# Performance work log

Hardware: AMD Instinct MI355X
Metric: run time of the kernel (lower is better)

## Reference

```python
import jax, jax.numpy as jnp
import numpy as np

T, B, E, H = 2048, 2, 1024, 16
HD = E // H
EPS = 1e-5


def setup_inputs() -> dict:
    key = jax.random.key(0)
    k1, k2, k3 = jax.random.split(key, 3)
    bound_in = float(np.sqrt(6.0 / (3 * E + E)))   # xavier_uniform for [3E,E]
    bound_out = float(np.sqrt(6.0 / (E + E)))      # xavier_uniform for [E,E]
    return {
        "query": jax.random.normal(k1, (T, B, E), dtype=jnp.float32),
        "gamma": jnp.ones((E,), dtype=jnp.float32),
        "beta": jnp.zeros((E,), dtype=jnp.float32),
        "in_proj_weight": jax.random.uniform(k2, (3 * E, E), jnp.float32, -bound_in, bound_in),
        "out_proj_weight": jax.random.uniform(k3, (E, E), jnp.float32, -bound_out, bound_out),
    }


def reference(query, gamma, beta, in_proj_weight, out_proj_weight):
    # LayerNorm over channel dim
    mean = jnp.mean(query, axis=-1, keepdims=True)
    var = jnp.mean(jnp.square(query - mean), axis=-1, keepdims=True)
    ln = (query - mean) * jax.lax.rsqrt(var + EPS) * gamma + beta  # [T,B,E]

    # Fused QKV projection (no bias): qkv = ln @ W^T, W: [3E, E]
    qkv = jnp.einsum("tbe,fe->tbf", ln, in_proj_weight)  # [T,B,3E]
    q, k, v = jnp.split(qkv, 3, axis=-1)
    q = q.reshape(T, B, H, HD) * (HD ** -0.5)
    k = k.reshape(T, B, H, HD)
    v = v.reshape(T, B, H, HD)

    # Attention: scores [B,H,T,T]
    scores = jnp.einsum("tbhd,sbhd->bhts", q, k)
    attn = jax.nn.softmax(scores, axis=-1)
    ctx = jnp.einsum("bhts,sbhd->tbhd", attn, v).reshape(T, B, E)

    # Output projection + residual add (dropout prob = 0)
    out = jnp.einsum("tbe,fe->tbf", ctx, out_proj_weight)
    return query + out
```

## Files before the change

kernel.cpp:

```cpp
#include <hip/hip_runtime.h>
#include <hip/hip_bf16.h>
#include <math.h>

#define T_DIM 2048
#define B_DIM 2
#define E_DIM 1024
#define H_DIM 16
#define HD_DIM 64
#define M_DIM (T_DIM * B_DIM)
#define BH_DIM (B_DIM * H_DIM)

using bf16x8 = __attribute__((ext_vector_type(8))) __bf16;
using u16x8  = __attribute__((ext_vector_type(8))) unsigned short;
using u16x4  = __attribute__((ext_vector_type(4))) unsigned short;
using f32x4  = __attribute__((ext_vector_type(4))) float;

static __device__ __forceinline__ unsigned short f2bf(float f) {
  unsigned u = __builtin_bit_cast(unsigned, f);
  u += 0x7fff + ((u >> 16) & 1);
  return (unsigned short)(u >> 16);
}

__device__ __forceinline__ void gload_lds16(const void* g, void* l) {
  __builtin_amdgcn_global_load_lds(
      (const __attribute__((address_space(1))) unsigned int*)g,
      (__attribute__((address_space(3))) unsigned int*)l, 16, 0, 0);
}

__global__ __launch_bounds__(256) void cast2_kernel(
    const float* __restrict__ in1, unsigned short* __restrict__ out1, int n1,
    const float* __restrict__ in2, unsigned short* __restrict__ out2, int n2) {
  int i = blockIdx.x * 256 + threadIdx.x;
  const float* in; unsigned short* out; int idx;
  if (i < n1) { in = in1; out = out1; idx = i; }
  else if (i < n1 + n2) { in = in2; out = out2; idx = i - n1; }
  else return;
  float4 v = ((const float4*)in)[idx];
  ushort4 o;
  o.x = f2bf(v.x); o.y = f2bf(v.y); o.z = f2bf(v.z); o.w = f2bf(v.w);
  ((ushort4*)out)[idx] = o;
}

__global__ __launch_bounds__(256) void ln_kernel(
    const float* __restrict__ q, const float* __restrict__ gamma,
    const float* __restrict__ beta, unsigned short* __restrict__ out) {
  int row = blockIdx.x;
  int tid = threadIdx.x;
  const float4* qr = (const float4*)(q + (size_t)row * E_DIM);
  float4 x = qr[tid];
  float s  = x.x + x.y + x.z + x.w;
  float ss = x.x * x.x + x.y * x.y + x.z * x.z + x.w * x.w;
#pragma unroll
  for (int off = 32; off >= 1; off >>= 1) {
    s  += __shfl_xor(s, off, 64);
    ss += __shfl_xor(ss, off, 64);
  }
  __shared__ float red[8];
  int wid = tid >> 6, lane = tid & 63;
  if (lane == 0) { red[wid] = s; red[4 + wid] = ss; }
  __syncthreads();
  s  = red[0] + red[1] + red[2] + red[3];
  ss = red[4] + red[5] + red[6] + red[7];
  float mean = s * (1.0f / E_DIM);
  float var  = ss * (1.0f / E_DIM) - mean * mean;
  float rstd = rsqrtf(var + 1e-5f);
  float4 g4 = ((const float4*)gamma)[tid];
  float4 b4 = ((const float4*)beta)[tid];
  ushort4 o;
  o.x = f2bf((x.x - mean) * rstd * g4.x + b4.x);
  o.y = f2bf((x.y - mean) * rstd * g4.y + b4.y);
  o.z = f2bf((x.z - mean) * rstd * g4.z + b4.z);
  o.w = f2bf((x.w - mean) * rstd * g4.w + b4.w);
  ((ushort4*)(out + (size_t)row * E_DIM))[tid] = o;
}

__global__ __launch_bounds__(256) void gemm0_kernel(
    const unsigned short* __restrict__ A, const unsigned short* __restrict__ Bw,
    unsigned short* __restrict__ out_qkv) {
  __shared__ alignas(16) unsigned short lA[128 * 32];
  __shared__ alignas(16) unsigned short lB[128 * 32];
  int tid = threadIdx.x;
  int wid = tid >> 6, lane = tid & 63;
  int wm = wid >> 1, wn = wid & 1;
  int g = lane >> 4, lr = lane & 15;
  int m0 = blockIdx.y * 128, n0 = blockIdx.x * 128;
  f32x4 acc[4][4] = {};

  for (int k0 = 0; k0 < E_DIM; k0 += 32) {
#pragma unroll
    for (int c = 0; c < 2; ++c) {
      int f16 = c * 256 + tid;
      int row = f16 >> 2, col8 = (f16 & 3) << 3;
      gload_lds16(A  + (size_t)(m0 + row) * E_DIM + k0 + col8,
                  lA + (size_t)(c * 256 + wid * 64) * 8);
      gload_lds16(Bw + (size_t)(n0 + row) * E_DIM + k0 + col8,
                  lB + (size_t)(c * 256 + wid * 64) * 8);
    }
    __syncthreads();
    bf16x8 af[4], bfr[4];
#pragma unroll
    for (int r = 0; r < 4; ++r) {
      af[r]  = *(const bf16x8*)(lA + (wm * 64 + r * 16 + lr) * 32 + g * 8);
      bfr[r] = *(const bf16x8*)(lB + (wn * 64 + r * 16 + lr) * 32 + g * 8);
    }
#pragma unroll
    for (int mr = 0; mr < 4; ++mr)
#pragma unroll
      for (int nr = 0; nr < 4; ++nr)
        acc[mr][nr] = __builtin_amdgcn_mfma_f32_16x16x32_bf16(
            af[mr], bfr[nr], acc[mr][nr], 0, 0, 0);
    __syncthreads();
  }

#pragma unroll
  for (int mr = 0; mr < 4; ++mr) {
#pragma unroll
    for (int nr = 0; nr < 4; ++nr) {
#pragma unroll
      for (int r = 0; r < 4; ++r) {
        int grow = m0 + wm * 64 + mr * 16 + g * 4 + r;
        int gcol = n0 + wn * 64 + nr * 16 + lr;
        int which = gcol >> 10, rem = gcol & 1023;
        int h = rem >> 6, d = rem & 63;
        int t = grow >> 1, b = grow & 1;
        out_qkv[(size_t)which * (BH_DIM * T_DIM * HD_DIM) +
                ((size_t)(b * H_DIM + h) * T_DIM + t) * HD_DIM + d] =
            f2bf(acc[mr][nr][r]);
      }
    }
  }
}

__global__ __launch_bounds__(256) void gemm1_kernel(
    const unsigned short* __restrict__ A, const unsigned short* __restrict__ Bw,
    const float* __restrict__ resid, float* __restrict__ out) {
  __shared__ alignas(16) unsigned short lA[128 * 32];
  __shared__ alignas(16) unsigned short lB[64 * 32];
  int tid = threadIdx.x;
  int wid = tid >> 6, lane = tid & 63;
  int g = lane >> 4, lr = lane & 15;
  int m0 = blockIdx.y * 128, n0 = blockIdx.x * 64;
  f32x4 acc[2][4] = {};

  for (int k0 = 0; k0 < E_DIM; k0 += 32) {
#pragma unroll
    for (int c = 0; c < 2; ++c) {
      int f16 = c * 256 + tid;
      int row = f16 >> 2, col8 = (f16 & 3) << 3;
      gload_lds16(A + (size_t)(m0 + row) * E_DIM + k0 + col8,
                  lA + (size_t)(c * 256 + wid * 64) * 8);
    }
    {
      int row = tid >> 2, col8 = (tid & 3) << 3;
      gload_lds16(Bw + (size_t)(n0 + row) * E_DIM + k0 + col8,
                  lB + (size_t)(wid * 64) * 8);
    }
    __syncthreads();
    bf16x8 af[2], bfr[4];
#pragma unroll
    for (int r = 0; r < 2; ++r)
      af[r] = *(const bf16x8*)(lA + (wid * 32 + r * 16 + lr) * 32 + g * 8);
#pragma unroll
    for (int r = 0; r < 4; ++r)
      bfr[r] = *(const bf16x8*)(lB + (r * 16 + lr) * 32 + g * 8);
#pragma unroll
    for (int mr = 0; mr < 2; ++mr)
#pragma unroll
      for (int nr = 0; nr < 4; ++nr)
        acc[mr][nr] = __builtin_amdgcn_mfma_f32_16x16x32_bf16(
            af[mr], bfr[nr], acc[mr][nr], 0, 0, 0);
    __syncthreads();
  }

#pragma unroll
  for (int mr = 0; mr < 2; ++mr) {
#pragma unroll
    for (int nr = 0; nr < 4; ++nr) {
#pragma unroll
      for (int r = 0; r < 4; ++r) {
        int grow = m0 + wid * 32 + mr * 16 + g * 4 + r;
        int gcol = n0 + nr * 16 + lr;
        size_t idx = (size_t)grow * E_DIM + gcol;
        out[idx] = resid[idx] + acc[mr][nr][r];
      }
    }
  }
}

__global__ __launch_bounds__(256) void transpose_v_kernel(
    const unsigned short* __restrict__ vb, unsigned short* __restrict__ vt) {
  __shared__ alignas(16) unsigned short tl[64 * 72];
  int tid = threadIdx.x;
  int bh = blockIdx.y, t0 = blockIdx.x * 64;
  const unsigned short* src = vb + ((size_t)bh * T_DIM + t0) * HD_DIM;
#pragma unroll
  for (int e = 0; e < 2; ++e) {
    int i8 = e * 256 + tid;
    int r = i8 >> 3;
    int c = (i8 & 7) * 8;
    int hsh = (r ^ (r >> 3)) & 7;
    bf16x8 v = *(const bf16x8*)(src + (size_t)r * HD_DIM + c);
    *(bf16x8*)(tl + r * 72 + (c ^ (hsh << 3))) = v;
  }
  __syncthreads();
  unsigned short* dst = vt + (size_t)bh * HD_DIM * T_DIM + t0;
#pragma unroll
  for (int e = 0; e < 2; ++e) {
    int i8 = e * 256 + tid;
    int d = i8 >> 3;
    int tc = (i8 & 7) * 8;
    u16x8 o;
#pragma unroll
    for (int j = 0; j < 8; ++j) {
      int p = tc + j;
      int ks = p >> 5, gg = (p >> 3) & 3, jl = p & 7;
      int r = (ks * 2 + (jl >> 2)) * 16 + gg * 4 + (jl & 3);
      int hsh = (r ^ (r >> 3)) & 7;
      o[j] = tl[r * 72 + (d ^ (hsh << 3))];
    }
    *(u16x8*)(dst + (size_t)d * T_DIM + tc) = o;
  }
}

__global__ __launch_bounds__(256) void attn_kernel(
    const unsigned short* __restrict__ qb, const unsigned short* __restrict__ kb,
    const unsigned short* __restrict__ vt, unsigned short* __restrict__ ctx) {
  __shared__ alignas(16) unsigned short lK[3][64 * 64];
  __shared__ alignas(16) unsigned short lV[3][64 * 64];
  int tid = threadIdx.x;
  int wid = tid >> 6, lane = tid & 63;
  int g = lane >> 4, lr = lane & 15;
  int f = blockIdx.x;
  int xcd = f & 7, rest = f >> 3;
  int bh = xcd + 8 * (rest & 3);
  int qt = rest >> 2;
  int b = bh >> 4, h = bh & 15;
  const size_t koff = (size_t)bh * T_DIM * HD_DIM;
  const size_t voff = (size_t)bh * HD_DIM * T_DIM;

  int srow = tid >> 3;
  int gch  = (tid & 7) ^ (srow & 7);
  const unsigned short* ks0 = kb + koff + (size_t)srow * HD_DIM + gch * 8;
  const unsigned short* vs0 = vt + voff + (size_t)srow * T_DIM + gch * 8;

#define STAGE_TILE(buf, kofs, vofs)                                            \
  do {                                                                         \
    gload_lds16(ks0 + (kofs),                 lK[buf] + wid * 512);            \
    gload_lds16(ks0 + (kofs) + 32 * HD_DIM,   lK[buf] + 2048 + wid * 512);     \
    gload_lds16(vs0 + (vofs),                 lV[buf] + wid * 512);            \
    gload_lds16(vs0 + (vofs) + (size_t)32 * T_DIM, lV[buf] + 2048 + wid * 512);\
  } while (0)

  bf16x8 qf[2][2];
  {
    const float QS = 0.125f * 1.44269504f;
#pragma unroll
    for (int qa = 0; qa < 2; ++qa) {
      int qrow = qt * 128 + wid * 32 + qa * 16 + lr;
#pragma unroll
      for (int ks = 0; ks < 2; ++ks) {
        bf16x8 raw = *(const bf16x8*)(qb + koff + (size_t)qrow * HD_DIM + ks * 32 + g * 8);
#pragma unroll
        for (int j = 0; j < 8; ++j) qf[qa][ks][j] = (__bf16)((float)raw[j] * QS);
      }
    }
  }

  bf16x8 onesf;
#pragma unroll
  for (int j = 0; j < 8; ++j) onesf[j] = (__bf16)1.0f;

  f32x4 accO[2][4] = {};
  f32x4 accS[2] = {};

  const int NT = T_DIM / 64;
  STAGE_TILE(0, 0, 0);

#define PROCESS(BUF, NBUF, TT, LAST)                                           \
  do {                                                                         \
    if (!(LAST)) {                                                             \
      size_t s1 = (size_t)((TT) + 1) * 64;                                     \
      STAGE_TILE(NBUF, s1 * HD_DIM, s1);                                       \
      asm volatile("s_waitcnt vmcnt(4)" ::: "memory");                         \
    } else {                                                                   \
      asm volatile("s_waitcnt vmcnt(0)" ::: "memory");                         \
    }                                                                          \
    __builtin_amdgcn_s_barrier();                                              \
    __builtin_amdgcn_sched_barrier(0);                                         \
    const unsigned short* Kc = lK[BUF];                                        \
    const unsigned short* Vc = lV[BUF];                                        \
    f32x4 s4[2][4];                                                            \
    __builtin_amdgcn_s_setprio(1);                                             \
    _Pragma("unroll")                                                          \
    for (int cf = 0; cf < 4; ++cf) {                                           \
      int row = cf * 16 + lr;                                                  \
      int sw = (row & 7) << 3;                                                 \
      bf16x8 k0 = *(const bf16x8*)(Kc + row * 64 + ((g * 8) ^ sw));            \
      bf16x8 k1 = *(const bf16x8*)(Kc + row * 64 + ((32 + g * 8) ^ sw));       \
      _Pragma("unroll")                                                        \
      for (int qa = 0; qa < 2; ++qa) {                                         \
        f32x4 s = {-8.0f, -8.0f, -8.0f, -8.0f};                                \
        s = __builtin_amdgcn_mfma_f32_16x16x32_bf16(k0, qf[qa][0], s, 0, 0, 0);\
        s = __builtin_amdgcn_mfma_f32_16x16x32_bf16(k1, qf[qa][1], s, 0, 0, 0);\
        s4[qa][cf] = s;                                                        \
      }                                                                        \
    }                                                                          \
    __builtin_amdgcn_s_setprio(0);                                             \
    bf16x8 pf[2][2];                                                           \
    _Pragma("unroll")                                                          \
    for (int qa = 0; qa < 2; ++qa)                                             \
      _Pragma("unroll")                                                        \
      for (int j = 0; j < 8; ++j) {                                            \
        pf[qa][0][j] = (__bf16)__builtin_amdgcn_exp2f(s4[qa][(j >> 2)][j & 3]);\
        pf[qa][1][j] = (__bf16)__builtin_amdgcn_exp2f(s4[qa][2 + (j >> 2)][j & 3]);\
      }                                                                        \
    __builtin_amdgcn_s_setprio(1);                                             \
    _Pragma("unroll")                                                          \
    for (int ks = 0; ks < 2; ++ks) {                                           \
      _Pragma("unroll")                                                        \
      for (int qa = 0; qa < 2; ++qa)                                           \
        accS[qa] = __builtin_amdgcn_mfma_f32_16x16x32_bf16(onesf, pf[qa][ks], accS[qa], 0, 0, 0); \
      _Pragma("unroll")                                                        \
      for (int df = 0; df < 4; ++df) {                                         \
        int row = df * 16 + lr;                                                \
        int sw = (row & 7) << 3;                                               \
        bf16x8 vf = *(const bf16x8*)(Vc + row * 64 + ((ks * 32 + g * 8) ^ sw));\
        _Pragma("unroll")                                                      \
        for (int qa = 0; qa < 2; ++qa)                                         \
          accO[qa][df] = __builtin_amdgcn_mfma_f32_16x16x32_bf16(vf, pf[qa][ks], accO[qa][df], 0, 0, 0); \
      }                                                                        \
    }                                                                          \
    __builtin_amdgcn_s_setprio(0);                                             \
  } while (0)

  for (int t3 = 0; t3 < 30; t3 += 3) {
    PROCESS(0, 1, t3 + 0, false);
    PROCESS(1, 2, t3 + 1, false);
    PROCESS(2, 0, t3 + 2, false);
  }
  PROCESS(0, 1, 30, false);
  PROCESS(1, 2, 31, true);
#undef PROCESS
#undef STAGE_TILE

  __syncthreads();
  unsigned short* sc = (unsigned short*)lK + wid * (32 * 72);
  float invl[2];
  invl[0] = 1.0f / accS[0][0];
  invl[1] = 1.0f / accS[1][0];
#pragma unroll
  for (int qa = 0; qa < 2; ++qa)
#pragma unroll
    for (int df = 0; df < 4; ++df)
#pragma unroll
      for (int r = 0; r < 4; ++r)
        sc[(qa * 16 + lr) * 72 + df * 16 + g * 4 + r] =
            f2bf(accO[qa][df][r] * invl[qa]);
  __syncthreads();
#pragma unroll
  for (int i = 0; i < 4; ++i) {
    int idx = i * 64 + lane;
    int row = idx >> 3, ch = idx & 7;
    u16x8 v8 = *(const u16x8*)(sc + row * 72 + ch * 8);
    int t = qt * 128 + wid * 32 + row;
    *(u16x8*)(&ctx[((size_t)t * B_DIM + b) * E_DIM + h * HD_DIM + ch * 8]) = v8;
  }
}

extern "C" void kernel_launch(void* const* d_in, const int* in_sizes, int n_in,
                              void* d_out, int out_size, void* d_ws, size_t ws_size,
                              hipStream_t stream) {
  const float* query = (const float*)d_in[0];
  const float* gamma = (const float*)d_in[1];
  const float* beta  = (const float*)d_in[2];
  const float* w_in  = (const float*)d_in[3];
  const float* w_out = (const float*)d_in[4];
  float* out = (float*)d_out;

  unsigned short* ws    = (unsigned short*)d_ws;
  unsigned short* ln    = ws;
  unsigned short* winb  = ln + (size_t)M_DIM * E_DIM;
  unsigned short* woutb = winb + (size_t)3 * E_DIM * E_DIM;
  unsigned short* qkv   = woutb + (size_t)E_DIM * E_DIM;

  unsigned short* qbuf = qkv;
  unsigned short* kbuf = qkv + (size_t)BH_DIM * T_DIM * HD_DIM;
  unsigned short* vbuf = kbuf + (size_t)BH_DIM * T_DIM * HD_DIM;
  unsigned short* vtb  = ln;
  unsigned short* ctx  = vbuf;

  cast2_kernel<<<dim3(4096), dim3(256), 0, stream>>>(
      w_in, winb, 3 * E_DIM * E_DIM / 4, w_out, woutb, E_DIM * E_DIM / 4);
  ln_kernel<<<dim3(M_DIM), dim3(256), 0, stream>>>(query, gamma, beta, ln);
  gemm0_kernel<<<dim3(3 * E_DIM / 128, M_DIM / 128), dim3(256), 0, stream>>>(
      ln, winb, qkv);
  transpose_v_kernel<<<dim3(T_DIM / 64, BH_DIM), dim3(256), 0, stream>>>(vbuf, vtb);
  attn_kernel<<<dim3(512), dim3(256), 0, stream>>>(qbuf, kbuf, vtb, ctx);
  gemm1_kernel<<<dim3(E_DIM / 64, M_DIM / 128), dim3(256), 0, stream>>>(
      ctx, woutb, query, out);
}
```

Before: 122.3 us.

## Split attention over key halves with reduce kernel; fuse V transpose into QKV GEMM

```diff
diff --git a/kernel.cpp b/kernel.cpp
--- a/kernel.cpp
+++ b/kernel.cpp
@@ -12,13 +12,15 @@
 
 using bf16x8 = __attribute__((ext_vector_type(8))) __bf16;
 using u16x8  = __attribute__((ext_vector_type(8))) unsigned short;
-using u16x4  = __attribute__((ext_vector_type(4))) unsigned short;
 using f32x4  = __attribute__((ext_vector_type(4))) float;
 
 static __device__ __forceinline__ unsigned short f2bf(float f) {
   unsigned u = __builtin_bit_cast(unsigned, f);
   u += 0x7fff + ((u >> 16) & 1);
   return (unsigned short)(u >> 16);
+}
+static __device__ __forceinline__ float bf2f(unsigned short x) {
+  return __builtin_bit_cast(float, (unsigned)x << 16);
 }
 
 __device__ __forceinline__ void gload_lds16(const void* g, void* l) {
@@ -76,7 +78,8 @@
 
 __global__ __launch_bounds__(256) void gemm0_kernel(
     const unsigned short* __restrict__ A, const unsigned short* __restrict__ Bw,
-    unsigned short* __restrict__ out_qkv) {
+    unsigned short* __restrict__ out_q, unsigned short* __restrict__ out_k,
+    unsigned short* __restrict__ out_vt) {
   __shared__ alignas(16) unsigned short lA[128 * 32];
   __shared__ alignas(16) unsigned short lB[128 * 32];
   int tid = threadIdx.x;
@@ -123,9 +126,19 @@
         int which = gcol >> 10, rem = gcol & 1023;
         int h = rem >> 6, d = rem & 63;
         int t = grow >> 1, b = grow & 1;
-        out_qkv[(size_t)which * (BH_DIM * T_DIM * HD_DIM) +
-                ((size_t)(b * H_DIM + h) * T_DIM + t) * HD_DIM + d] =
-            f2bf(acc[mr][nr][r]);
+        size_t bh = (size_t)(b * H_DIM + h);
+        unsigned short val = f2bf(acc[mr][nr][r]);
+        if (which == 0) {
+          out_q[(bh * T_DIM + t) * HD_DIM + d] = val;
+        } else if (which == 1) {
+          out_k[(bh * T_DIM + t) * HD_DIM + d] = val;
+        } else {
+          int tile = t >> 6, trow = t & 63;
+          int cf = trow >> 4, rr = trow & 15;
+          int ks2 = cf >> 1, jh = cf & 1, g2 = rr >> 2, jl = rr & 3;
+          int p = ks2 * 32 + g2 * 8 + jh * 4 + jl;
+          out_vt[bh * (HD_DIM * T_DIM) + (size_t)d * T_DIM + tile * 64 + p] = val;
+        }
       }
     }
   }
@@ -187,61 +200,29 @@
   }
 }
 
-__global__ __launch_bounds__(256) void transpose_v_kernel(
-    const unsigned short* __restrict__ vb, unsigned short* __restrict__ vt) {
-  __shared__ alignas(16) unsigned short tl[64 * 72];
-  int tid = threadIdx.x;
-  int bh = blockIdx.y, t0 = blockIdx.x * 64;
-  const unsigned short* src = vb + ((size_t)bh * T_DIM + t0) * HD_DIM;
-#pragma unroll
-  for (int e = 0; e < 2; ++e) {
-    int i8 = e * 256 + tid;
-    int r = i8 >> 3;
-    int c = (i8 & 7) * 8;
-    int hsh = (r ^ (r >> 3)) & 7;
-    bf16x8 v = *(const bf16x8*)(src + (size_t)r * HD_DIM + c);
-    *(bf16x8*)(tl + r * 72 + (c ^ (hsh << 3))) = v;
-  }
-  __syncthreads();
-  unsigned short* dst = vt + (size_t)bh * HD_DIM * T_DIM + t0;
-#pragma unroll
-  for (int e = 0; e < 2; ++e) {
-    int i8 = e * 256 + tid;
-    int d = i8 >> 3;
-    int tc = (i8 & 7) * 8;
-    u16x8 o;
-#pragma unroll
-    for (int j = 0; j < 8; ++j) {
-      int p = tc + j;
-      int ks = p >> 5, gg = (p >> 3) & 3, jl = p & 7;
-      int r = (ks * 2 + (jl >> 2)) * 16 + gg * 4 + (jl & 3);
-      int hsh = (r ^ (r >> 3)) & 7;
-      o[j] = tl[r * 72 + (d ^ (hsh << 3))];
-    }
-    *(u16x8*)(dst + (size_t)d * T_DIM + tc) = o;
-  }
-}
-
 __global__ __launch_bounds__(256) void attn_kernel(
     const unsigned short* __restrict__ qb, const unsigned short* __restrict__ kb,
-    const unsigned short* __restrict__ vt, unsigned short* __restrict__ ctx) {
-  __shared__ alignas(16) unsigned short lK[3][64 * 64];
-  __shared__ alignas(16) unsigned short lV[3][64 * 64];
+    const unsigned short* __restrict__ vt, unsigned short* __restrict__ pO,
+    float* __restrict__ pS) {
+  __shared__ alignas(16) unsigned short lK[2][64 * 64];
+  __shared__ alignas(16) unsigned short lV[2][64 * 64];
   int tid = threadIdx.x;
   int wid = tid >> 6, lane = tid & 63;
   int g = lane >> 4, lr = lane & 15;
   int f = blockIdx.x;
   int xcd = f & 7, rest = f >> 3;
   int bh = xcd + 8 * (rest & 3);
-  int qt = rest >> 2;
-  int b = bh >> 4, h = bh & 15;
+  int qt = (rest >> 2) & 15;
+  int s  = (rest >> 6) & 1;
   const size_t koff = (size_t)bh * T_DIM * HD_DIM;
   const size_t voff = (size_t)bh * HD_DIM * T_DIM;
 
   int srow = tid >> 3;
   int gch  = (tid & 7) ^ (srow & 7);
-  const unsigned short* ks0 = kb + koff + (size_t)srow * HD_DIM + gch * 8;
-  const unsigned short* vs0 = vt + voff + (size_t)srow * T_DIM + gch * 8;
+  const unsigned short* ks0 = kb + koff +
+      ((size_t)(s * 1024) + srow) * HD_DIM + gch * 8;
+  const unsigned short* vs0 = vt + voff +
+      (size_t)srow * T_DIM + s * 1024 + gch * 8;
 
 #define STAGE_TILE(buf, kofs, vofs)                                            \
   do {                                                                         \
@@ -273,19 +254,19 @@
   f32x4 accO[2][4] = {};
   f32x4 accS[2] = {};
 
-  const int NT = T_DIM / 64;
   STAGE_TILE(0, 0, 0);
 
-#define PROCESS(BUF, NBUF, TT, LAST)                                           \
+#define PROCESS(BUF, TT, LAST)                                                 \
   do {                                                                         \
+    __builtin_amdgcn_s_barrier();            \
     if (!(LAST)) {                                                             \
       size_t s1 = (size_t)((TT) + 1) * 64;                                     \
-      STAGE_TILE(NBUF, s1 * HD_DIM, s1);                                       \
+      STAGE_TILE((BUF) ^ 1, s1 * HD_DIM, s1);                                  \
       asm volatile("s_waitcnt vmcnt(4)" ::: "memory");                         \
     } else {                                                                   \
       asm volatile("s_waitcnt vmcnt(0)" ::: "memory");                         \
     }                                                                          \
-    __builtin_amdgcn_s_barrier();                                              \
+    __builtin_amdgcn_s_barrier();              \
     __builtin_amdgcn_sched_barrier(0);                                         \
     const unsigned short* Kc = lK[BUF];                                        \
     const unsigned short* Vc = lV[BUF];                                        \
@@ -333,38 +314,67 @@
     __builtin_amdgcn_s_setprio(0);                                             \
   } while (0)
 
-  for (int t3 = 0; t3 < 30; t3 += 3) {
-    PROCESS(0, 1, t3 + 0, false);
-    PROCESS(1, 2, t3 + 1, false);
-    PROCESS(2, 0, t3 + 2, false);
-  }
-  PROCESS(0, 1, 30, false);
-  PROCESS(1, 2, 31, true);
+  for (int t2 = 0; t2 < 16; t2 += 2) {
+    PROCESS(0, t2, false);
+    PROCESS(1, t2 + 1, t2 + 1 == 15);
+  }
 #undef PROCESS
 #undef STAGE_TILE
 
+  unsigned short* pOb = pO + (size_t)((s * 32 + bh) * 16 + qt) * (64 * 128);
+#pragma unroll
+  for (int qa = 0; qa < 2; ++qa)
+#pragma unroll
+    for (int df = 0; df < 4; ++df)
+#pragma unroll
+      for (int r = 0; r < 4; ++r)
+        pOb[(df * 16 + g * 4 + r) * 128 + wid * 32 + qa * 16 + lr] =
+            f2bf(accO[qa][df][r]);
+  if (g == 0) {
+    float* pSb = pS + (size_t)((s * 32 + bh) * 16 + qt) * 128;
+#pragma unroll
+    for (int qa = 0; qa < 2; ++qa)
+      pSb[wid * 32 + qa * 16 + lr] = accS[qa][0];
+  }
+}
+
+__global__ __launch_bounds__(256) void reduce_kernel(
+    const unsigned short* __restrict__ pO, const float* __restrict__ pS,
+    unsigned short* __restrict__ ctx) {
+  __shared__ float lo[64][65];
+  __shared__ float ls[64];
+  int tid = threadIdx.x;
+  int bq = blockIdx.x;
+  int bh = bq & 31, qt2 = bq >> 5;
+  int b = bh >> 4, h = bh & 15;
+  int qt = qt2 >> 1, half = qt2 & 1;
+  size_t base0 = (size_t)((0 * 32 + bh) * 16 + qt) * 8192 + half * 64;
+  size_t base1 = (size_t)((1 * 32 + bh) * 16 + qt) * 8192 + half * 64;
+  int d = tid >> 2, c = (tid & 3) * 16;
+  u16x8 a0 = *(const u16x8*)(pO + base0 + d * 128 + c);
+  u16x8 a1 = *(const u16x8*)(pO + base0 + d * 128 + c + 8);
+  u16x8 b0 = *(const u16x8*)(pO + base1 + d * 128 + c);
+  u16x8 b1 = *(const u16x8*)(pO + base1 + d * 128 + c + 8);
+#pragma unroll
+  for (int j = 0; j < 8; ++j) {
+    lo[d][c + j]     = bf2f(a0[j]) + bf2f(b0[j]);
+    lo[d][c + 8 + j] = bf2f(a1[j]) + bf2f(b1[j]);
+  }
+  if (tid < 64)
+    ls[tid] = pS[(size_t)((0 * 32 + bh) * 16 + qt) * 128 + half * 64 + tid] +
+              pS[(size_t)((1 * 32 + bh) * 16 + qt) * 128 + half * 64 + tid];
   __syncthreads();
-  unsigned short* sc = (unsigned short*)lK + wid * (32 * 72);
-  float invl[2];
-  invl[0] = 1.0f / accS[0][0];
-  invl[1] = 1.0f / accS[1][0];
-#pragma unroll
-  for (int qa = 0; qa < 2; ++qa)
-#pragma unroll
-    for (int df = 0; df < 4; ++df)
-#pragma unroll
-      for (int r = 0; r < 4; ++r)
-        sc[(qa * 16 + lr) * 72 + df * 16 + g * 4 + r] =
-            f2bf(accO[qa][df][r] * invl[qa]);
-  __syncthreads();
-#pragma unroll
-  for (int i = 0; i < 4; ++i) {
-    int idx = i * 64 + lane;
-    int row = idx >> 3, ch = idx & 7;
-    u16x8 v8 = *(const u16x8*)(sc + row * 72 + ch * 8);
-    int t = qt * 128 + wid * 32 + row;
-    *(u16x8*)(&ctx[((size_t)t * B_DIM + b) * E_DIM + h * HD_DIM + ch * 8]) = v8;
-  }
+  int q = tid >> 2, dc = tid & 3;
+  float inv = 1.0f / ls[q];
+  u16x8 o0, o1;
+#pragma unroll
+  for (int k = 0; k < 8; ++k) {
+    o0[k] = f2bf(lo[dc * 16 + k][q] * inv);
+    o1[k] = f2bf(lo[dc * 16 + 8 + k][q] * inv);
+  }
+  size_t row = ((size_t)(qt2 * 64 + q) * B_DIM + b) * E_DIM + h * HD_DIM + dc * 16;
+  *(u16x8*)(ctx + row)     = o0;
+  *(u16x8*)(ctx + row + 8) = o1;
 }
 
 extern "C" void kernel_launch(void* const* d_in, const int* in_sizes, int n_in,
@@ -379,23 +389,22 @@
 
   unsigned short* ws    = (unsigned short*)d_ws;
   unsigned short* ln    = ws;
-  unsigned short* winb  = ln + (size_t)M_DIM * E_DIM;
-  unsigned short* woutb = winb + (size_t)3 * E_DIM * E_DIM;
-  unsigned short* qkv   = woutb + (size_t)E_DIM * E_DIM;
-
-  unsigned short* qbuf = qkv;
-  unsigned short* kbuf = qkv + (size_t)BH_DIM * T_DIM * HD_DIM;
-  unsigned short* vbuf = kbuf + (size_t)BH_DIM * T_DIM * HD_DIM;
-  unsigned short* vtb  = ln;
-  unsigned short* ctx  = vbuf;
+  unsigned short* winb  = ln    + (size_t)M_DIM * E_DIM;
+  unsigned short* woutb = winb  + (size_t)3 * E_DIM * E_DIM;
+  unsigned short* qbuf  = woutb + (size_t)E_DIM * E_DIM;
+  unsigned short* kbuf  = qbuf  + (size_t)BH_DIM * T_DIM * HD_DIM;
+  unsigned short* vtb   = kbuf  + (size_t)BH_DIM * T_DIM * HD_DIM;
+  unsigned short* pO    = vtb   + (size_t)BH_DIM * HD_DIM * T_DIM;
+  float*          pS    = (float*)(pO + (size_t)2 * BH_DIM * 16 * 64 * 128);
+  unsigned short* ctx   = ln;
 
   cast2_kernel<<<dim3(4096), dim3(256), 0, stream>>>(
       w_in, winb, 3 * E_DIM * E_DIM / 4, w_out, woutb, E_DIM * E_DIM / 4);
   ln_kernel<<<dim3(M_DIM), dim3(256), 0, stream>>>(query, gamma, beta, ln);
   gemm0_kernel<<<dim3(3 * E_DIM / 128, M_DIM / 128), dim3(256), 0, stream>>>(
-      ln, winb, qkv);
-  transpose_v_kernel<<<dim3(T_DIM / 64, BH_DIM), dim3(256), 0, stream>>>(vbuf, vtb);
-  attn_kernel<<<dim3(512), dim3(256), 0, stream>>>(qbuf, kbuf, vtb, ctx);
+      ln, winb, qbuf, kbuf, vtb);
+  attn_kernel<<<dim3(1024), dim3(256), 0, stream>>>(qbuf, kbuf, vtb, pO, pS);
+  reduce_kernel<<<dim3(1024), dim3(256), 0, stream>>>(pO, pS, ctx);
   gemm1_kernel<<<dim3(E_DIM / 64, M_DIM / 128), dim3(256), 0, stream>>>(
       ctx, woutb, query, out);
 }
```

Result: slower. 149.2 us (+22.0%).

## Software-pipeline QK^T of next tile with PV of current tile; merge prep kernels

Applied to the files above, without the earlier changes.

```diff
diff --git a/kernel.cpp b/kernel.cpp
--- a/kernel.cpp
+++ b/kernel.cpp
@@ -12,7 +12,6 @@
 
 using bf16x8 = __attribute__((ext_vector_type(8))) __bf16;
 using u16x8  = __attribute__((ext_vector_type(8))) unsigned short;
-using u16x4  = __attribute__((ext_vector_type(4))) unsigned short;
 using f32x4  = __attribute__((ext_vector_type(4))) float;
 
 static __device__ __forceinline__ unsigned short f2bf(float f) {
@@ -27,25 +26,26 @@
       (__attribute__((address_space(3))) unsigned int*)l, 16, 0, 0);
 }
 
-__global__ __launch_bounds__(256) void cast2_kernel(
-    const float* __restrict__ in1, unsigned short* __restrict__ out1, int n1,
-    const float* __restrict__ in2, unsigned short* __restrict__ out2, int n2) {
-  int i = blockIdx.x * 256 + threadIdx.x;
-  const float* in; unsigned short* out; int idx;
-  if (i < n1) { in = in1; out = out1; idx = i; }
-  else if (i < n1 + n2) { in = in2; out = out2; idx = i - n1; }
-  else return;
-  float4 v = ((const float4*)in)[idx];
-  ushort4 o;
-  o.x = f2bf(v.x); o.y = f2bf(v.y); o.z = f2bf(v.z); o.w = f2bf(v.w);
-  ((ushort4*)out)[idx] = o;
-}
-
-__global__ __launch_bounds__(256) void ln_kernel(
+__global__ __launch_bounds__(256) void prep_kernel(
     const float* __restrict__ q, const float* __restrict__ gamma,
-    const float* __restrict__ beta, unsigned short* __restrict__ out) {
-  int row = blockIdx.x;
+    const float* __restrict__ beta, unsigned short* __restrict__ ln_out,
+    const float* __restrict__ w1, unsigned short* __restrict__ o1, int n1,
+    const float* __restrict__ w2, unsigned short* __restrict__ o2, int n2) {
+  int blk = blockIdx.x;
   int tid = threadIdx.x;
+  if (blk >= M_DIM) {
+    int i = (blk - M_DIM) * 256 + tid;
+    const float* in; unsigned short* out; int idx;
+    if (i < n1) { in = w1; out = o1; idx = i; }
+    else if (i < n1 + n2) { in = w2; out = o2; idx = i - n1; }
+    else return;
+    float4 v = ((const float4*)in)[idx];
+    ushort4 o;
+    o.x = f2bf(v.x); o.y = f2bf(v.y); o.z = f2bf(v.z); o.w = f2bf(v.w);
+    ((ushort4*)out)[idx] = o;
+    return;
+  }
+  int row = blk;
   const float4* qr = (const float4*)(q + (size_t)row * E_DIM);
   float4 x = qr[tid];
   float s  = x.x + x.y + x.z + x.w;
@@ -71,7 +71,7 @@
   o.y = f2bf((x.y - mean) * rstd * g4.y + b4.y);
   o.z = f2bf((x.z - mean) * rstd * g4.z + b4.z);
   o.w = f2bf((x.w - mean) * rstd * g4.w + b4.w);
-  ((ushort4*)(out + (size_t)row * E_DIM))[tid] = o;
+  ((ushort4*)(ln_out + (size_t)row * E_DIM))[tid] = o;
 }
 
 __global__ __launch_bounds__(256) void gemm0_kernel(
@@ -272,25 +272,11 @@
 
   f32x4 accO[2][4] = {};
   f32x4 accS[2] = {};
-
-  const int NT = T_DIM / 64;
-  STAGE_TILE(0, 0, 0);
-
-#define PROCESS(BUF, NBUF, TT, LAST)                                           \
+  f32x4 s4c[2][4];
+
+#define QK_TILE(BUF, S4)                                                       \
   do {                                                                         \
-    if (!(LAST)) {                                                             \
-      size_t s1 = (size_t)((TT) + 1) * 64;                                     \
-      STAGE_TILE(NBUF, s1 * HD_DIM, s1);                                       \
-      asm volatile("s_waitcnt vmcnt(4)" ::: "memory");                         \
-    } else {                                                                   \
-      asm volatile("s_waitcnt vmcnt(0)" ::: "memory");                         \
-    }                                                                          \
-    __builtin_amdgcn_s_barrier();                                              \
-    __builtin_amdgcn_sched_barrier(0);                                         \
     const unsigned short* Kc = lK[BUF];                                        \
-    const unsigned short* Vc = lV[BUF];                                        \
-    f32x4 s4[2][4];                                                            \
-    __builtin_amdgcn_s_setprio(1);                                             \
     _Pragma("unroll")                                                          \
     for (int cf = 0; cf < 4; ++cf) {                                           \
       int row = cf * 16 + lr;                                                  \
@@ -302,45 +288,75 @@
         f32x4 s = {-8.0f, -8.0f, -8.0f, -8.0f};                                \
         s = __builtin_amdgcn_mfma_f32_16x16x32_bf16(k0, qf[qa][0], s, 0, 0, 0);\
         s = __builtin_amdgcn_mfma_f32_16x16x32_bf16(k1, qf[qa][1], s, 0, 0, 0);\
-        s4[qa][cf] = s;                                                        \
+        S4[qa][cf] = s;                                                        \
       }                                                                        \
     }                                                                          \
-    __builtin_amdgcn_s_setprio(0);                                             \
+  } while (0)
+
+  STAGE_TILE(0, 0, 0);
+  STAGE_TILE(1, (size_t)64 * HD_DIM, 64);
+  asm volatile("s_waitcnt vmcnt(4)" ::: "memory");
+  __builtin_amdgcn_s_barrier();
+  __builtin_amdgcn_sched_barrier(0);
+  QK_TILE(0, s4c);
+
+#define PROCESS(B0, B1, B2, TT, STG, QKN)                                      \
+  do {                                                                         \
+    asm volatile("s_waitcnt vmcnt(0)" ::: "memory");                           \
+    __builtin_amdgcn_s_barrier();                                              \
+    __builtin_amdgcn_sched_barrier(0);                                         \
+    if (STG) {                                                                 \
+      size_t s2 = (size_t)((TT) + 2) * 64;                                     \
+      STAGE_TILE(B2, s2 * HD_DIM, s2);                                         \
+    }                                                                          \
+    __builtin_amdgcn_s_setprio(1);                                             \
+    f32x4 s4n[2][4];                                                           \
+    if (QKN) QK_TILE(B1, s4n);                                                 \
     bf16x8 pf[2][2];                                                           \
     _Pragma("unroll")                                                          \
     for (int qa = 0; qa < 2; ++qa)                                             \
       _Pragma("unroll")                                                        \
       for (int j = 0; j < 8; ++j) {                                            \
-        pf[qa][0][j] = (__bf16)__builtin_amdgcn_exp2f(s4[qa][(j >> 2)][j & 3]);\
-        pf[qa][1][j] = (__bf16)__builtin_amdgcn_exp2f(s4[qa][2 + (j >> 2)][j & 3]);\
+        pf[qa][0][j] = (__bf16)__builtin_amdgcn_exp2f(s4c[qa][(j >> 2)][j & 3]);\
+        pf[qa][1][j] = (__bf16)__builtin_amdgcn_exp2f(s4c[qa][2 + (j >> 2)][j & 3]);\
       }                                                                        \
-    __builtin_amdgcn_s_setprio(1);                                             \
-    _Pragma("unroll")                                                          \
-    for (int ks = 0; ks < 2; ++ks) {                                           \
+    {                                                                          \
+      const unsigned short* Vc = lV[B0];                                       \
       _Pragma("unroll")                                                        \
-      for (int qa = 0; qa < 2; ++qa)                                           \
-        accS[qa] = __builtin_amdgcn_mfma_f32_16x16x32_bf16(onesf, pf[qa][ks], accS[qa], 0, 0, 0); \
-      _Pragma("unroll")                                                        \
-      for (int df = 0; df < 4; ++df) {                                         \
-        int row = df * 16 + lr;                                                \
-        int sw = (row & 7) << 3;                                               \
-        bf16x8 vf = *(const bf16x8*)(Vc + row * 64 + ((ks * 32 + g * 8) ^ sw));\
+      for (int ks = 0; ks < 2; ++ks) {                                         \
         _Pragma("unroll")                                                      \
         for (int qa = 0; qa < 2; ++qa)                                         \
-          accO[qa][df] = __builtin_amdgcn_mfma_f32_16x16x32_bf16(vf, pf[qa][ks], accO[qa][df], 0, 0, 0); \
+          accS[qa] = __builtin_amdgcn_mfma_f32_16x16x32_bf16(onesf, pf[qa][ks], accS[qa], 0, 0, 0); \
+        _Pragma("unroll")                                                      \
+        for (int df = 0; df < 4; ++df) {                                       \
+          int row = df * 16 + lr;                                              \
+          int sw = (row & 7) << 3;                                             \
+          bf16x8 vf = *(const bf16x8*)(Vc + row * 64 + ((ks * 32 + g * 8) ^ sw));\
+          _Pragma("unroll")                                                    \
+          for (int qa = 0; qa < 2; ++qa)                                       \
+            accO[qa][df] = __builtin_amdgcn_mfma_f32_16x16x32_bf16(vf, pf[qa][ks], accO[qa][df], 0, 0, 0); \
+        }                                                                      \
       }                                                                        \
     }                                                                          \
     __builtin_amdgcn_s_setprio(0);                                             \
+    if (QKN) {                                                                 \
+      _Pragma("unroll")                                                        \
+      for (int qa = 0; qa < 2; ++qa)                                           \
+        _Pragma("unroll")                                                      \
+        for (int cf = 0; cf < 4; ++cf)                                         \
+          s4c[qa][cf] = s4n[qa][cf];                                           \
+    }                                                                          \
   } while (0)
 
   for (int t3 = 0; t3 < 30; t3 += 3) {
-    PROCESS(0, 1, t3 + 0, false);
-    PROCESS(1, 2, t3 + 1, false);
-    PROCESS(2, 0, t3 + 2, false);
-  }
-  PROCESS(0, 1, 30, false);
-  PROCESS(1, 2, 31, true);
+    PROCESS(0, 1, 2, t3 + 0, true, true);
+    PROCESS(1, 2, 0, t3 + 1, true, true);
+    PROCESS(2, 0, 1, t3 + 2, true, true);
+  }
+  PROCESS(0, 1, 2, 30, false, true);
+  PROCESS(1, 2, 0, 31, false, false);
 #undef PROCESS
+#undef QK_TILE
 #undef STAGE_TILE
 
   __syncthreads();
@@ -389,9 +405,9 @@
   unsigned short* vtb  = ln;
   unsigned short* ctx  = vbuf;
 
-  cast2_kernel<<<dim3(4096), dim3(256), 0, stream>>>(
+  prep_kernel<<<dim3(M_DIM + 4096), dim3(256), 0, stream>>>(
+      query, gamma, beta, ln,
       w_in, winb, 3 * E_DIM * E_DIM / 4, w_out, woutb, E_DIM * E_DIM / 4);
-  ln_kernel<<<dim3(M_DIM), dim3(256), 0, stream>>>(query, gamma, beta, ln);
   gemm0_kernel<<<dim3(3 * E_DIM / 128, M_DIM / 128), dim3(256), 0, stream>>>(
       ln, winb, qkv);
   transpose_v_kernel<<<dim3(T_DIM / 64, BH_DIM), dim3(256), 0, stream>>>(vbuf, vtb);
```

Measured after the change: 121.9 us. Within noise of the previous version (-0.3%).
